# Performance work log

Measured on AMD Instinct MI355X. Metric: run time of the kernel, lower is better.

## Reference

```python
import jax, jax.numpy as jnp
import numpy as np
from jax import lax

B, T, D = 2, 2048, 2048
H, DK, DV = 16, 128, 128
K = 4  # conv kernel size
KEY_DIM = H * DK      # 2048
VAL_DIM = H * DV      # 2048
CONV_DIM = 2 * KEY_DIM + VAL_DIM  # 6144
EPS = 1e-6


def setup_inputs() -> dict:
    key = jax.random.key(0)
    ks = jax.random.split(key, 10)
    s = lambda fan: 1.0 / np.sqrt(fan)
    return {
        "hidden_states": jax.random.normal(ks[0], (B, T, D), jnp.float32),
        "W_qkv": jax.random.normal(ks[1], (D, CONV_DIM), jnp.float32) * s(D),
        "conv_w": jax.random.normal(ks[2], (CONV_DIM, 1, K), jnp.float32) * s(K),
        "W_z": jax.random.normal(ks[3], (D, VAL_DIM), jnp.float32) * s(D),
        "W_b": jax.random.normal(ks[4], (D, H), jnp.float32) * s(D),
        "W_a": jax.random.normal(ks[5], (D, H), jnp.float32) * s(D),
        "dt_bias": jnp.ones((H,), jnp.float32),
        "A_log": jnp.log(jax.random.uniform(ks[6], (H,), jnp.float32, 1e-3, 16.0)),
        "norm_weight": jnp.ones((DV,), jnp.float32),
        "W_out": jax.random.normal(ks[7], (VAL_DIM, D), jnp.float32) * s(VAL_DIM),
    }


def _l2norm(x):
    return x * lax.rsqrt(jnp.sum(x * x, axis=-1, keepdims=True) + 1e-6)


def _gated_delta_rule(q, k, v, g, beta):
    """q,k: [B,T,H,DK]; v: [B,T,H,DV]; g,beta: [B,T,H]. Returns o: [B,T,H,DV]."""
    # time-major for scan
    qT, kT, vT = (jnp.moveaxis(x, 1, 0) for x in (q, k, v))  # [T,B,H,d]
    gT = jnp.moveaxis(g, 1, 0)      # [T,B,H]
    bT = jnp.moveaxis(beta, 1, 0)   # [T,B,H]

    def step(S, inp):
        q_t, k_t, v_t, g_t, b_t = inp
        S = S * jnp.exp(g_t)[..., None, None]                      # decay [B,H,DK,DV]
        kv_mem = jnp.einsum("bhk,bhkv->bhv", k_t, S)               # S^T k
        delta = (v_t - kv_mem) * b_t[..., None]                     # beta-scaled error
        S = S + jnp.einsum("bhk,bhv->bhkv", k_t, delta)
        o_t = jnp.einsum("bhk,bhkv->bhv", q_t, S)
        return S, o_t

    S0 = jnp.zeros((q.shape[0], H, DK, DV), q.dtype)
    _, oT = lax.scan(step, S0, (qT, kT, vT, gT, bT))
    return jnp.moveaxis(oT, 0, 1)  # [B,T,H,DV]


def reference(hidden_states, W_qkv, conv_w, W_z, W_b, W_a, dt_bias, A_log,
              norm_weight, W_out):
    Bs, Ts, _ = hidden_states.shape

    # qkv projection + depthwise causal conv1d + silu
    mixed = hidden_states @ W_qkv                      # [B,T,CONV_DIM]
    xc = jnp.moveaxis(mixed, 1, 2)                     # [B,C,T]
    xc = lax.conv_general_dilated(xc, conv_w, (1,), [(K - 1, 0)],
                                  feature_group_count=CONV_DIM)
    mixed = jax.nn.silu(jnp.moveaxis(xc, 1, 2))        # [B,T,C]

    q, k, v = jnp.split(mixed, [KEY_DIM, 2 * KEY_DIM], axis=-1)
    q = _l2norm(q.reshape(Bs, Ts, H, DK)) * (DK ** -0.5)
    k = _l2norm(k.reshape(Bs, Ts, H, DK))
    v = v.reshape(Bs, Ts, H, DV)

    beta = jax.nn.sigmoid(hidden_states @ W_b)                     # [B,T,H]
    g = -jnp.exp(A_log) * jax.nn.softplus(hidden_states @ W_a + dt_bias)

    o = _gated_delta_rule(q, k, v, g, beta)            # [B,T,H,DV]

    # gated RMSNorm (Mamba2-style: gate first, then normalize)
    z = (hidden_states @ W_z).reshape(Bs, Ts, H, DV)
    o = o * jax.nn.silu(z)
    var = jnp.mean(o * o, axis=-1, keepdims=True)
    o = o * lax.rsqrt(var + EPS) * norm_weight

    return o.reshape(Bs, Ts, VAL_DIM) @ W_out          # [B,T,D]
```

## Files before the change

### kernel.cpp

```cpp
#include <hip/hip_runtime.h>

#define B_ 2
#define T_ 2048
#define D_ 2048
#define H_ 16
#define CONV_DIM_ 6144
#define NC_ 32
#define CK_ 64

typedef __bf16 bf16;
typedef bf16 bf16x8 __attribute__((ext_vector_type(8)));
typedef bf16 bf16x4 __attribute__((ext_vector_type(4)));
typedef float floatx4 __attribute__((ext_vector_type(4)));

__device__ __forceinline__ void async_copy16(bf16* lds, const bf16* g) {
    auto* g1 = (const __attribute__((address_space(1))) unsigned int*)g;
    auto* l3 = (__attribute__((address_space(3))) unsigned int*)lds;
    __builtin_amdgcn_global_load_lds(g1, l3, 16, 0, 0);
}

__global__ void cvt_bf16_kernel(const float* __restrict__ in, bf16* __restrict__ out, int n4) {
    int i = blockIdx.x * 256 + threadIdx.x;
    if (i < n4) {
        float4 v = ((const float4*)in)[i];
        bf16x4 o = { (bf16)v.x, (bf16)v.y, (bf16)v.z, (bf16)v.w };
        *(bf16x4*)(out + 4 * (size_t)i) = o;
    }
}

__global__ void transpose_kernel(const float* __restrict__ in, bf16* __restrict__ out, int R, int Cn) {
    __shared__ float tile[32][33];
    const int c0 = blockIdx.x << 5, r0 = blockIdx.y << 5;
    const int tx = threadIdx.x & 31, ty = threadIdx.x >> 5;
#pragma unroll
    for (int i = 0; i < 4; ++i) {
        int r = ty + (i << 3);
        tile[r][tx] = in[(size_t)(r0 + r) * Cn + c0 + tx];
    }
    __syncthreads();
#pragma unroll
    for (int i = 0; i < 4; ++i) {
        int cc = ty + (i << 3);
        out[(size_t)(c0 + cc) * R + r0 + tx] = (bf16)tile[tx][cc];
    }
}

__global__ void wba_cvt_kernel(const float* __restrict__ Wb, const float* __restrict__ Wa,
                               bf16* __restrict__ Wba) {
    int idx = blockIdx.x * 256 + threadIdx.x;
    int d = idx >> 4, h = idx & 15;
    Wba[(size_t)h * 2048 + d]        = (bf16)Wb[idx];
    Wba[(size_t)(h + 16) * 2048 + d] = (bf16)Wa[idx];
}

template <typename OutT>
__global__ __launch_bounds__(256) void gemm_kernel(
    const bf16* __restrict__ A, const bf16* __restrict__ Bt, OutT* __restrict__ C,
    int M, int N, int K) {
    __shared__ bf16 As[128 * 64];
    __shared__ bf16 Bs[128 * 64];
    const int tid = threadIdx.x;
    const int m0 = blockIdx.y << 7;
    const int n0 = blockIdx.x << 7;
    const int wave = tid >> 6, lane = tid & 63;
    const int wm = (wave >> 1) << 6, wn = (wave & 1) << 6;
    const int lrow = lane & 15, quad = lane >> 4;
    const int rl = lane >> 3;
    const int c8s = (lane & 7) ^ (rl & 7);

    floatx4 acc[4][4];
#pragma unroll
    for (int mt = 0; mt < 4; ++mt)
#pragma unroll
        for (int nt = 0; nt < 4; ++nt)
            acc[mt][nt] = floatx4{0.f, 0.f, 0.f, 0.f};

    for (int k0 = 0; k0 < K; k0 += 64) {
        __syncthreads();
#pragma unroll
        for (int i = 0; i < 4; ++i) {
            const int slot = wave * 4 + i;
            const int r = slot * 8 + rl;
            async_copy16(&As[slot * 512], A + (size_t)(m0 + r) * K + k0 + c8s * 8);
            async_copy16(&Bs[slot * 512], Bt + (size_t)(n0 + r) * K + k0 + c8s * 8);
        }
        __syncthreads();
#pragma unroll
        for (int kk = 0; kk < 64; kk += 32) {
            const int sw = (((kk >> 3) + quad) ^ (lrow & 7)) << 3;
            bf16x8 af[4], bfr[4];
#pragma unroll
            for (int mt = 0; mt < 4; ++mt) {
                af[mt]  = *(const bf16x8*)(&As[((wm + (mt << 4) + lrow) << 6) + sw]);
                bfr[mt] = *(const bf16x8*)(&Bs[((wn + (mt << 4) + lrow) << 6) + sw]);
            }
#pragma unroll
            for (int mt = 0; mt < 4; ++mt)
#pragma unroll
                for (int nt = 0; nt < 4; ++nt)
                    acc[mt][nt] = __builtin_amdgcn_mfma_f32_16x16x32_bf16(af[mt], bfr[nt], acc[mt][nt], 0, 0, 0);
        }
    }
#pragma unroll
    for (int mt = 0; mt < 4; ++mt)
#pragma unroll
        for (int nt = 0; nt < 4; ++nt) {
            const int col = n0 + wn + (nt << 4) + lrow;
            const int rowb = m0 + wm + (mt << 4) + (quad << 2);
#pragma unroll
            for (int i2 = 0; i2 < 4; ++i2)
                C[(size_t)(rowb + i2) * N + col] = (OutT)acc[mt][nt][i2];
        }
}

__global__ void conv_silu_kernel(const bf16* __restrict__ mixed, const float* __restrict__ cw,
                                 bf16* __restrict__ qb, bf16* __restrict__ kb, bf16* __restrict__ vb) {
    const int s = blockIdx.x;
    const int bt = blockIdx.y;
    const int t = bt & (T_ - 1);
    const int b = bt >> 11;
    const int c = (s << 7) + threadIdx.x;
    const size_t base = (size_t)bt * CONV_DIM_ + c;
    const float w0 = cw[c * 4], w1 = cw[c * 4 + 1], w2 = cw[c * 4 + 2], w3 = cw[c * 4 + 3];
    float acc = (float)mixed[base] * w3;
    if (t >= 1) acc += (float)mixed[base - CONV_DIM_] * w2;
    if (t >= 2) acc += (float)mixed[base - 2 * CONV_DIM_] * w1;
    if (t >= 3) acc += (float)mixed[base - 3 * CONV_DIM_] * w0;
    const float val = acc / (1.f + __expf(-acc));

    __shared__ float red[2];
    if (s < 32) {
        float ss = val * val;
#pragma unroll
        for (int o = 1; o < 64; o <<= 1) ss += __shfl_xor(ss, o);
        if ((threadIdx.x & 63) == 0) red[threadIdx.x >> 6] = ss;
        __syncthreads();
        const float scale = rsqrtf(red[0] + red[1] + 1e-6f);
        const int h = s & 15;
        const size_t oidx = (((size_t)(b * H_ + h)) * T_ + t) * 128 + threadIdx.x;
        if (s < 16) qb[oidx] = (bf16)(val * scale * 0.08838834764831845f);
        else        kb[oidx] = (bf16)(val * scale);
    } else {
        const int h = s - 32;
        const size_t oidx = (((size_t)(b * H_ + h)) * T_ + t) * 128 + threadIdx.x;
        vb[oidx] = (bf16)val;
    }
}

__global__ __launch_bounds__(256) void gbeta_mfma_kernel(
    const bf16* __restrict__ Xb, const bf16* __restrict__ Wba,
    const float* __restrict__ dtb, const float* __restrict__ Alog,
    float* __restrict__ gbuf, float* __restrict__ bbuf) {
    const int tid = threadIdx.x, wave = tid >> 6, lane = tid & 63;
    const int ln = lane & 15, qd = lane >> 4;
    const int m0 = blockIdx.x * 64 + wave * 16;
    floatx4 acc0 = {0.f, 0.f, 0.f, 0.f}, acc1 = {0.f, 0.f, 0.f, 0.f};
    const bf16* arow = Xb + (size_t)(m0 + ln) * 2048 + qd * 8;
    const bf16* b0 = Wba + (size_t)ln * 2048 + qd * 8;
    const bf16* b1 = Wba + (size_t)(16 + ln) * 2048 + qd * 8;
    for (int k = 0; k < 2048; k += 32) {
        bf16x8 af  = *(const bf16x8*)(arow + k);
        bf16x8 bf0 = *(const bf16x8*)(b0 + k);
        bf16x8 bf1 = *(const bf16x8*)(b1 + k);
        acc0 = __builtin_amdgcn_mfma_f32_16x16x32_bf16(af, bf0, acc0, 0, 0, 0);
        acc1 = __builtin_amdgcn_mfma_f32_16x16x32_bf16(af, bf1, acc1, 0, 0, 0);
    }
    const float dtbv = dtb[ln], al = __expf(Alog[ln]);
#pragma unroll
    for (int ii = 0; ii < 4; ++ii) {
        const int row = m0 + qd * 4 + ii;
        const int t = row & (T_ - 1), b = row >> 11;
        const size_t o = ((size_t)(b * H_ + ln)) * T_ + t;
        bbuf[o] = 1.f / (1.f + __expf(-acc0[ii]));
        const float xx = acc1[ii] + dtbv;
        const float sp = (xx > 15.f) ? xx : log1pf(__expf(xx));
        gbuf[o] = -al * sp;
    }
}

__global__ __launch_bounds__(256) void qkkt_kernel(const bf16* __restrict__ qb, const bf16* __restrict__ kb,
                                                   float* __restrict__ Araw, float* __restrict__ Mraw) {
    const int u = blockIdx.x;
    const int bh = u >> 5, nc = u & 31;
    const int t0 = nc * CK_;
    const int tid = threadIdx.x, wave = tid >> 6, lane = tid & 63;
    const int qd = lane >> 4, ln = lane & 15;
    __shared__ bf16 Kc[64 * 136], Qc[64 * 136];
    const size_t kbase = ((size_t)bh * T_ + t0) * 128;
#pragma unroll
    for (int it = 0; it < 4; ++it) {
        int idx = it * 256 + tid;
        int row = idx >> 4, c8 = idx & 15;
        *(uint4*)(&Kc[row * 136 + c8 * 8]) = *(const uint4*)(kb + kbase + row * 128 + c8 * 8);
        *(uint4*)(&Qc[row * 136 + c8 * 8]) = *(const uint4*)(qb + kbase + row * 128 + c8 * 8);
    }
    __syncthreads();
#pragma unroll
    for (int nt = 0; nt < 4; ++nt) {
        floatx4 accA = {0.f, 0.f, 0.f, 0.f}, accM = {0.f, 0.f, 0.f, 0.f};
#pragma unroll
        for (int kk = 0; kk < 4; ++kk) {
            bf16x8 bfr = *(const bf16x8*)(&Kc[(nt * 16 + ln) * 136 + kk * 32 + qd * 8]);
            bf16x8 afK = *(const bf16x8*)(&Kc[(wave * 16 + ln) * 136 + kk * 32 + qd * 8]);
            bf16x8 afQ = *(const bf16x8*)(&Qc[(wave * 16 + ln) * 136 + kk * 32 + qd * 8]);
            accA = __builtin_amdgcn_mfma_f32_16x16x32_bf16(afK, bfr, accA, 0, 0, 0);
            accM = __builtin_amdgcn_mfma_f32_16x16x32_bf16(afQ, bfr, accM, 0, 0, 0);
        }
#pragma unroll
        for (int ii = 0; ii < 4; ++ii) {
            int i = wave * 16 + qd * 4 + ii, j = nt * 16 + ln;
            Araw[(size_t)u * 4096 + i * 64 + j] = accA[ii];
            Mraw[(size_t)u * 4096 + i * 64 + j] = accM[ii];
        }
    }
}

__global__ __launch_bounds__(64) void prep_kernel(
    const float* __restrict__ gbuf, const float* __restrict__ bbuf,
    const float* __restrict__ Araw, const float* __restrict__ Mraw,
    float* __restrict__ lamg, float* __restrict__ ratiog,
    bf16* __restrict__ Tg, bf16* __restrict__ Mg) {
    const int u = blockIdx.x, bh = u >> 5, nc = u & 31, t0 = nc * CK_;
    const int lane = threadIdx.x;
    __shared__ float L[64 * 65];
    __shared__ float cv[64], bv[64];
    float g = gbuf[(size_t)bh * T_ + t0 + lane];
    float beta = bbuf[(size_t)bh * T_ + t0 + lane];
    float c = g;
#pragma unroll
    for (int off = 1; off < 64; off <<= 1) {
        float tval = __shfl_up(c, off);
        if (lane >= off) c += tval;
    }
    float c63 = __shfl(c, 63);
    lamg[(size_t)u * 64 + lane] = __expf(c);
    ratiog[(size_t)u * 64 + lane] = __expf(c63 - c);
    cv[lane] = c; bv[lane] = beta;
    __syncthreads();
    for (int i = 0; i < 64; ++i) {
        float a = Araw[(size_t)u * 4096 + i * 64 + lane];
        L[i * 65 + lane] = (lane < i) ? bv[i] * __expf(cv[i] - c) * a : 0.f;
    }
    __syncthreads();
    float t[64];
#pragma unroll
    for (int i = 0; i < 64; ++i) t[i] = (i == lane) ? 1.f : 0.f;
#pragma unroll
    for (int j = 0; j < 63; ++j) {
#pragma unroll
        for (int i = j + 1; i < 64; ++i)
            t[i] -= L[i * 65 + j] * t[j];
    }
#pragma unroll
    for (int i = 0; i < 64; ++i)
        Tg[(size_t)u * 4096 + i * 64 + lane] = (bf16)t[i];
    for (int i = 0; i < 64; ++i) {
        float m = Mraw[(size_t)u * 4096 + i * 64 + lane];
        float mij = (lane <= i) ? __expf(cv[i] - c) * m : 0.f;
        Mg[(size_t)u * 4096 + i * 64 + lane] = (bf16)mij;
    }
}

struct Pref {
    uint4 t2[2], m2[2];
    bf16x8 kf[4], qf[4];
    bf16x8 ktf[2][2];
    float rrv[4], vv[4], lam[4], bet[4], lamlast;
};

__device__ __forceinline__ void load_pref(
    Pref& p, int u, int t0, size_t kbase, int tid, int wave, int ln, int qd,
    int bh, int vbase,
    const bf16* __restrict__ qb, const bf16* __restrict__ kb, const bf16* __restrict__ vb,
    const bf16* __restrict__ Tg, const bf16* __restrict__ Mg,
    const float* __restrict__ lamg, const float* __restrict__ ratiog,
    const float* __restrict__ bbuf) {
#pragma unroll
    for (int it = 0; it < 2; ++it) {
        int idx = it * 256 + tid;
        int row = idx >> 3, c8 = idx & 7;
        p.t2[it] = *(const uint4*)(Tg + (size_t)u * 4096 + row * 64 + c8 * 8);
        p.m2[it] = *(const uint4*)(Mg + (size_t)u * 4096 + row * 64 + c8 * 8);
    }
    const size_t rowoff = kbase + (size_t)(wave * 16 + ln) * 128;
#pragma unroll
    for (int kk = 0; kk < 4; ++kk) {
        p.kf[kk] = *(const bf16x8*)(kb + rowoff + kk * 32 + qd * 8);
        p.qf[kk] = *(const bf16x8*)(qb + rowoff + kk * 32 + qd * 8);
    }
#pragma unroll
    for (int mt = 0; mt < 2; ++mt) {
        const int kd = (wave * 2 + mt) * 16 + ln;
#pragma unroll
        for (int kk2 = 0; kk2 < 2; ++kk2) {
            const int ib = kk2 * 32 + qd * 8;
#pragma unroll
            for (int j = 0; j < 8; ++j)
                p.ktf[mt][kk2][j] = kb[kbase + (size_t)(ib + j) * 128 + kd];
        }
    }
    const int i0 = wave * 16 + qd * 4;
#pragma unroll
    for (int ii = 0; ii < 4; ++ii) {
        p.vv[ii]  = (float)vb[kbase + (size_t)(i0 + ii) * 128 + vbase + ln];
        p.lam[ii] = lamg[(size_t)u * 64 + i0 + ii];
        p.bet[ii] = bbuf[(size_t)bh * T_ + t0 + i0 + ii];
        p.rrv[ii] = ratiog[(size_t)u * 64 + i0 + ii];
    }
    p.lamlast = lamg[(size_t)u * 64 + 63];
}

__global__ __launch_bounds__(256) void seq_kernel(
    const bf16* __restrict__ qb, const bf16* __restrict__ kb, const bf16* __restrict__ vb,
    const bf16* __restrict__ Tg, const bf16* __restrict__ Mg,
    const float* __restrict__ lamg, const float* __restrict__ ratiog,
    const float* __restrict__ bbuf, float* __restrict__ ob) {
    const int bh = blockIdx.x & 31;
    const int vs = blockIdx.x >> 5;
    const int vbase = vs * 16;
    const int tid = threadIdx.x;
    const int wave = tid >> 6, lane = tid & 63;
    const int qd = lane >> 4, ln = lane & 15;

    __shared__ bf16 Tt[64 * 72], Mm[64 * 72];
    __shared__ bf16 bT[16 * 72], Dt[16 * 72], Dtr[16 * 72];
    __shared__ bf16 Sbf[16 * 136];
    __shared__ float Sf[16 * 132];

    for (int idx = tid; idx < 16 * 132; idx += 256) Sf[idx] = 0.f;
    for (int idx = tid; idx < 16 * 136; idx += 256) Sbf[idx] = (bf16)0.f;

    Pref cur, nxt;
    load_pref(cur, bh * NC_, 0, (size_t)bh * T_ * 128, tid, wave, ln, qd, bh, vbase,
              qb, kb, vb, Tg, Mg, lamg, ratiog, bbuf);
    __syncthreads();

    for (int nc = 0; nc < NC_; ++nc) {
        const int t0 = nc * CK_;
        const size_t kbase = ((size_t)bh * T_ + t0) * 128;

#pragma unroll
        for (int it = 0; it < 2; ++it) {
            int idx = it * 256 + tid;
            int row = idx >> 3, c8 = idx & 7;
            *(uint4*)(&Tt[row * 72 + c8 * 8]) = cur.t2[it];
            *(uint4*)(&Mm[row * 72 + c8 * 8]) = cur.m2[it];
        }

        {
            const int ncn = (nc + 1 < NC_) ? nc + 1 : nc;
            load_pref(nxt, bh * NC_ + ncn, ncn * CK_, ((size_t)bh * T_ + (size_t)ncn * CK_) * 128,
                      tid, wave, ln, qd, bh, vbase, qb, kb, vb, Tg, Mg, lamg, ratiog, bbuf);
        }

        floatx4 ks = {0.f, 0.f, 0.f, 0.f};
#pragma unroll
        for (int kk = 0; kk < 4; ++kk) {
            bf16x8 bf = *(const bf16x8*)(&Sbf[ln * 136 + kk * 32 + qd * 8]);
            ks = __builtin_amdgcn_mfma_f32_16x16x32_bf16(cur.kf[kk], bf, ks, 0, 0, 0);
        }
        {
            const int i0 = wave * 16 + qd * 4;
            bf16x4 bw;
#pragma unroll
            for (int ii = 0; ii < 4; ++ii)
                bw[ii] = (bf16)(cur.bet[ii] * (cur.vv[ii] - cur.lam[ii] * ks[ii]));
            *(bf16x4*)(&bT[ln * 72 + i0]) = bw;
        }
        __syncthreads();

        {
            floatx4 acc = {0.f, 0.f, 0.f, 0.f};
#pragma unroll
            for (int kk = 0; kk < 2; ++kk) {
                bf16x8 af = *(const bf16x8*)(&Tt[(wave * 16 + ln) * 72 + kk * 32 + qd * 8]);
                bf16x8 bf = *(const bf16x8*)(&bT[ln * 72 + kk * 32 + qd * 8]);
                acc = __builtin_amdgcn_mfma_f32_16x16x32_bf16(af, bf, acc, 0, 0, 0);
            }
            const int i0 = wave * 16 + qd * 4;
            bf16x4 dw = { (bf16)acc[0], (bf16)acc[1], (bf16)acc[2], (bf16)acc[3] };
            *(bf16x4*)(&Dt[ln * 72 + i0]) = dw;
            bf16x4 dwr = { (bf16)(acc[0] * cur.rrv[0]), (bf16)(acc[1] * cur.rrv[1]),
                           (bf16)(acc[2] * cur.rrv[2]), (bf16)(acc[3] * cur.rrv[3]) };
            *(bf16x4*)(&Dtr[ln * 72 + i0]) = dwr;
        }
        __syncthreads();

        {
            floatx4 acc = {0.f, 0.f, 0.f, 0.f};
#pragma unroll
            for (int kk = 0; kk < 4; ++kk) {
                bf16x8 bf = *(const bf16x8*)(&Sbf[ln * 136 + kk * 32 + qd * 8]);
                acc = __builtin_amdgcn_mfma_f32_16x16x32_bf16(cur.qf[kk], bf, acc, 0, 0, 0);
            }
            floatx4 o;
#pragma unroll
            for (int ii = 0; ii < 4; ++ii) o[ii] = acc[ii] * cur.lam[ii];
#pragma unroll
            for (int kk = 0; kk < 2; ++kk) {
                bf16x8 af = *(const bf16x8*)(&Mm[(wave * 16 + ln) * 72 + kk * 32 + qd * 8]);
                bf16x8 bf = *(const bf16x8*)(&Dt[ln * 72 + kk * 32 + qd * 8]);
                o = __builtin_amdgcn_mfma_f32_16x16x32_bf16(af, bf, o, 0, 0, 0);
            }
            const int i0 = wave * 16 + qd * 4;
#pragma unroll
            for (int ii = 0; ii < 4; ++ii)
                ob[kbase + (size_t)(i0 + ii) * 128 + vbase + ln] = o[ii];
        }
#pragma unroll
        for (int mt = 0; mt < 2; ++mt) {
            const int kt = wave * 2 + mt;
            floatx4 acc = {0.f, 0.f, 0.f, 0.f};
#pragma unroll
            for (int kk = 0; kk < 2; ++kk) {
                bf16x8 bf = *(const bf16x8*)(&Dtr[ln * 72 + kk * 32 + qd * 8]);
                acc = __builtin_amdgcn_mfma_f32_16x16x32_bf16(cur.ktf[mt][kk], bf, acc, 0, 0, 0);
            }
            const int k0 = kt * 16 + qd * 4;
            floatx4 sold = *(floatx4*)(&Sf[ln * 132 + k0]);
#pragma unroll
            for (int ii = 0; ii < 4; ++ii) sold[ii] = sold[ii] * cur.lamlast + acc[ii];
            *(floatx4*)(&Sf[ln * 132 + k0]) = sold;
        }
        __syncthreads();
        {
            const int vloc = tid >> 4, k0 = (tid & 15) * 8;
            floatx4 s0 = *(floatx4*)(&Sf[vloc * 132 + k0]);
            floatx4 s1 = *(floatx4*)(&Sf[vloc * 132 + k0 + 4]);
            bf16x8 sb = { (bf16)s0[0], (bf16)s0[1], (bf16)s0[2], (bf16)s0[3],
                          (bf16)s1[0], (bf16)s1[1], (bf16)s1[2], (bf16)s1[3] };
            *(bf16x8*)(&Sbf[vloc * 136 + k0]) = sb;
        }
        __syncthreads();
        cur = nxt;
    }
}

__global__ void gated_norm_kernel(const float* __restrict__ ob, const bf16* __restrict__ z,
                                  const float* __restrict__ nw, bf16* __restrict__ onorm) {
    const int idx = blockIdx.x;
    const int h = idx & (H_ - 1);
    const int bt = idx >> 4;
    const int t = bt & (T_ - 1);
    const int b = bt >> 11;
    const int tid = threadIdx.x;
    const size_t obase = (((size_t)(b * H_ + h)) * T_ + t) * 128;
    const size_t zbase = (size_t)bt * 2048 + (h << 7);
    float o1 = ob[obase + tid], o2 = ob[obase + tid + 64];
    const float z1 = (float)z[zbase + tid], z2 = (float)z[zbase + tid + 64];
    o1 *= z1 / (1.f + __expf(-z1));
    o2 *= z2 / (1.f + __expf(-z2));
    float ss = o1 * o1 + o2 * o2;
#pragma unroll
    for (int o = 1; o < 64; o <<= 1) ss += __shfl_xor(ss, o);
    const float scale = rsqrtf(ss * (1.f / 128.f) + 1e-6f);
    onorm[zbase + tid]      = (bf16)(o1 * scale * nw[tid]);
    onorm[zbase + tid + 64] = (bf16)(o2 * scale * nw[tid + 64]);
}

extern "C" void kernel_launch(void* const* d_in, const int* in_sizes, int n_in,
                              void* d_out, int out_size, void* d_ws, size_t ws_size,
                              hipStream_t stream) {
    const float* X    = (const float*)d_in[0];
    const float* Wqkv = (const float*)d_in[1];
    const float* cw   = (const float*)d_in[2];
    const float* Wz   = (const float*)d_in[3];
    const float* Wb   = (const float*)d_in[4];
    const float* Wa   = (const float*)d_in[5];
    const float* dtb  = (const float*)d_in[6];
    const float* Alog = (const float*)d_in[7];
    const float* nw   = (const float*)d_in[8];
    const float* Wout = (const float*)d_in[9];
    float* out = (float*)d_out;

    char* ws = (char*)d_ws;
    size_t off = 0;
    auto alloc = [&](size_t bytes) -> char* {
        char* p = ws + off;
        off += (bytes + 255) & ~(size_t)255;
        return p;
    };
    bf16*  Xb      = (bf16*)alloc((size_t)B_ * T_ * D_ * 2);
    char*  wqkvt_p = alloc((size_t)CONV_DIM_ * D_ * 2);
    bf16*  Wqkvt   = (bf16*)wqkvt_p;
    bf16*  Wzt     = (bf16*)alloc((size_t)D_ * D_ * 2);
    bf16*  Woutt   = (bf16*)alloc((size_t)D_ * D_ * 2);
    bf16*  Wba     = (bf16*)alloc((size_t)32 * 2048 * 2);
    char*  mixed_p = alloc((size_t)B_ * T_ * CONV_DIM_ * 2);
    bf16*  mixedb  = (bf16*)mixed_p;
    bf16*  zb      = (bf16*)alloc((size_t)B_ * T_ * D_ * 2);
    bf16*  kbuf    = (bf16*)alloc((size_t)B_ * T_ * D_ * 2);
    bf16*  vbuf    = (bf16*)alloc((size_t)B_ * T_ * D_ * 2);
    float* gbuf    = (float*)alloc((size_t)B_ * T_ * H_ * 4);
    float* bbuf    = (float*)alloc((size_t)B_ * T_ * H_ * 4);
    float* Mraw    = (float*)alloc((size_t)1024 * 4096 * 4);
    bf16*  Tg      = (bf16*)alloc((size_t)1024 * 4096 * 2);
    bf16*  Mg      = (bf16*)alloc((size_t)1024 * 4096 * 2);
    float* lamg    = (float*)alloc((size_t)1024 * 64 * 4);
    float* ratiog  = (float*)alloc((size_t)1024 * 64 * 4);
    bf16*  qbuf    = (bf16*)wqkvt_p;
    float* obuf    = (float*)mixed_p;
    float* Araw    = (float*)(mixed_p + (size_t)B_ * T_ * D_ * 4);
    bf16*  onorm   = (bf16*)Xb;

    cvt_bf16_kernel<<<dim3((B_ * T_ * D_ / 4 + 255) / 256), dim3(256), 0, stream>>>(X, Xb, B_ * T_ * D_ / 4);
    transpose_kernel<<<dim3(CONV_DIM_ / 32, D_ / 32), dim3(256), 0, stream>>>(Wqkv, Wqkvt, D_, CONV_DIM_);
    transpose_kernel<<<dim3(D_ / 32, D_ / 32), dim3(256), 0, stream>>>(Wz, Wzt, D_, D_);
    transpose_kernel<<<dim3(D_ / 32, D_ / 32), dim3(256), 0, stream>>>(Wout, Woutt, D_, D_);
    wba_cvt_kernel<<<dim3(128), dim3(256), 0, stream>>>(Wb, Wa, Wba);

    gemm_kernel<bf16><<<dim3(CONV_DIM_ / 128, B_ * T_ / 128), dim3(256), 0, stream>>>(
        Xb, Wqkvt, mixedb, B_ * T_, CONV_DIM_, D_);
    gemm_kernel<bf16><<<dim3(D_ / 128, B_ * T_ / 128), dim3(256), 0, stream>>>(
        Xb, Wzt, zb, B_ * T_, D_, D_);

    gbeta_mfma_kernel<<<dim3(64), dim3(256), 0, stream>>>(Xb, Wba, dtb, Alog, gbuf, bbuf);
    conv_silu_kernel<<<dim3(CONV_DIM_ / 128, B_ * T_), dim3(128), 0, stream>>>(mixedb, cw, qbuf, kbuf, vbuf);

    qkkt_kernel<<<dim3(1024), dim3(256), 0, stream>>>(qbuf, kbuf, Araw, Mraw);
    prep_kernel<<<dim3(1024), dim3(64), 0, stream>>>(gbuf, bbuf, Araw, Mraw, lamg, ratiog, Tg, Mg);
    seq_kernel<<<dim3(256), dim3(256), 0, stream>>>(qbuf, kbuf, vbuf, Tg, Mg, lamg, ratiog, bbuf, obuf);

    gated_norm_kernel<<<dim3(B_ * T_ * H_), dim3(64), 0, stream>>>(obuf, zb, nw, onorm);

    gemm_kernel<float><<<dim3(D_ / 128, B_ * T_ / 128), dim3(256), 0, stream>>>(
        onorm, Woutt, out, B_ * T_, D_, D_);
}
```

Baseline: 666.7 us.

## Merge QKV and Z projections into one 256x256-tiled double-buffered GEMM

The two input projection GEMMs (QKV and Z) are replaced by a single GEMM over a concatenated transposed weight of width 8192. The new kernel uses 256x256 tiles with 512 threads and double-buffered async global-to-LDS loads. Epilogue stores are routed to either the mixed buffer or the z buffer depending on the column block. The larger tiles raise arithmetic intensity and cut launches, but they use more LDS and registers, which could lower occupancy. The grid is also smaller, 32x16 blocks.

```diff
diff --git a/kernel.cpp b/kernel.cpp
--- a/kernel.cpp
+++ b/kernel.cpp
@@ -110,6 +110,101 @@
 #pragma unroll
             for (int i2 = 0; i2 < 4; ++i2)
                 C[(size_t)(rowb + i2) * N + col] = (OutT)acc[mt][nt][i2];
+        }
+}
+
+__global__ __launch_bounds__(512, 2) void gemm256_kernel(
+    const bf16* __restrict__ A, const bf16* __restrict__ Bt,
+    bf16* __restrict__ C0, bf16* __restrict__ C1,
+    int M, int Ncat, int K, int split, int ld0, int ld1) {
+    __shared__ bf16 As[2][256 * 64];
+    __shared__ bf16 Bs[2][256 * 64];
+    const int tid = threadIdx.x;
+    const int wave = tid >> 6, lane = tid & 63;
+    const int quad = lane >> 4, lrow = lane & 15;
+    const int wm = (wave >> 2) << 7;
+    const int wn = (wave & 3) << 6;
+    const int m0 = blockIdx.y << 8, n0 = blockIdx.x << 8;
+
+    const int srow = tid >> 3;
+    const int cu_src = (tid & 7) ^ (srow & 7);
+    const bf16* ga[4];
+    const bf16* gb[4];
+#pragma unroll
+    for (int i = 0; i < 4; ++i) {
+        ga[i] = A  + (size_t)(m0 + i * 64 + srow) * K + cu_src * 8;
+        gb[i] = Bt + (size_t)(n0 + i * 64 + srow) * K + cu_src * 8;
+    }
+
+    floatx4 acc[8][4];
+#pragma unroll
+    for (int mt = 0; mt < 8; ++mt)
+#pragma unroll
+        for (int nt = 0; nt < 4; ++nt)
+            acc[mt][nt] = floatx4{0.f, 0.f, 0.f, 0.f};
+
+    const int KT = K >> 6;
+    auto stage = [&](int b, int kt) {
+        const int k0 = kt << 6;
+#pragma unroll
+        for (int i = 0; i < 4; ++i) {
+            async_copy16(&As[b][i * 4096 + wave * 512], ga[i] + k0);
+            async_copy16(&Bs[b][i * 4096 + wave * 512], gb[i] + k0);
+        }
+    };
+    stage(0, 0);
+    stage(1, 1);
+
+    for (int kt = 0; kt < KT; ++kt) {
+        if (kt + 1 < KT) asm volatile("s_waitcnt vmcnt(8)" ::: "memory");
+        else             asm volatile("s_waitcnt vmcnt(0)" ::: "memory");
+        __builtin_amdgcn_sched_barrier(0);
+        __builtin_amdgcn_s_barrier();
+        __builtin_amdgcn_sched_barrier(0);
+        const bf16* as = &As[kt & 1][0];
+        const bf16* bs = &Bs[kt & 1][0];
+#pragma unroll
+        for (int kk = 0; kk < 2; ++kk) {
+            const int sw = (((kk << 2) + quad) ^ (lrow & 7)) << 3;
+            bf16x8 bfr[4];
+#pragma unroll
+            for (int nt = 0; nt < 4; ++nt)
+                bfr[nt] = *(const bf16x8*)(bs + ((wn + nt * 16 + lrow) << 6) + sw);
+#pragma unroll
+            for (int mh = 0; mh < 2; ++mh) {
+                bf16x8 af[4];
+#pragma unroll
+                for (int mt = 0; mt < 4; ++mt)
+                    af[mt] = *(const bf16x8*)(as + ((wm + (mh * 4 + mt) * 16 + lrow) << 6) + sw);
+                __builtin_amdgcn_s_setprio(1);
+#pragma unroll
+                for (int mt = 0; mt < 4; ++mt)
+#pragma unroll
+                    for (int nt = 0; nt < 4; ++nt)
+                        acc[mh * 4 + mt][nt] = __builtin_amdgcn_mfma_f32_16x16x32_bf16(
+                            af[mt], bfr[nt], acc[mh * 4 + mt][nt], 0, 0, 0);
+                __builtin_amdgcn_s_setprio(0);
+            }
+        }
+        __builtin_amdgcn_sched_barrier(0);
+        __builtin_amdgcn_s_barrier();
+        __builtin_amdgcn_sched_barrier(0);
+        if (kt + 2 < KT) stage(kt & 1, kt + 2);
+    }
+
+    const bool second = (n0 >= split);
+    bf16* Cp = second ? C1 : C0;
+    const int ldc = second ? ld1 : ld0;
+    const int nc0 = second ? n0 - split : n0;
+#pragma unroll
+    for (int mt = 0; mt < 8; ++mt)
+#pragma unroll
+        for (int nt = 0; nt < 4; ++nt) {
+            const int col = nc0 + wn + nt * 16 + lrow;
+            const int rowb = m0 + wm + mt * 16 + (quad << 2);
+#pragma unroll
+            for (int i2 = 0; i2 < 4; ++i2)
+                Cp[(size_t)(rowb + i2) * ldc + col] = (bf16)acc[mt][nt][i2];
         }
 }
 
@@ -481,9 +576,8 @@
         return p;
     };
     bf16*  Xb      = (bf16*)alloc((size_t)B_ * T_ * D_ * 2);
-    char*  wqkvt_p = alloc((size_t)CONV_DIM_ * D_ * 2);
-    bf16*  Wqkvt   = (bf16*)wqkvt_p;
-    bf16*  Wzt     = (bf16*)alloc((size_t)D_ * D_ * 2);
+    char*  wcat_p  = alloc((size_t)8192 * 2048 * 2);
+    bf16*  Wcat    = (bf16*)wcat_p;
     bf16*  Woutt   = (bf16*)alloc((size_t)D_ * D_ * 2);
     bf16*  Wba     = (bf16*)alloc((size_t)32 * 2048 * 2);
     char*  mixed_p = alloc((size_t)B_ * T_ * CONV_DIM_ * 2);
@@ -498,21 +592,19 @@
     bf16*  Mg      = (bf16*)alloc((size_t)1024 * 4096 * 2);
     float* lamg    = (float*)alloc((size_t)1024 * 64 * 4);
     float* ratiog  = (float*)alloc((size_t)1024 * 64 * 4);
-    bf16*  qbuf    = (bf16*)wqkvt_p;
+    bf16*  qbuf    = (bf16*)wcat_p;
     float* obuf    = (float*)mixed_p;
     float* Araw    = (float*)(mixed_p + (size_t)B_ * T_ * D_ * 4);
     bf16*  onorm   = (bf16*)Xb;
 
     cvt_bf16_kernel<<<dim3((B_ * T_ * D_ / 4 + 255) / 256), dim3(256), 0, stream>>>(X, Xb, B_ * T_ * D_ / 4);
-    transpose_kernel<<<dim3(CONV_DIM_ / 32, D_ / 32), dim3(256), 0, stream>>>(Wqkv, Wqkvt, D_, CONV_DIM_);
-    transpose_kernel<<<dim3(D_ / 32, D_ / 32), dim3(256), 0, stream>>>(Wz, Wzt, D_, D_);
+    transpose_kernel<<<dim3(CONV_DIM_ / 32, D_ / 32), dim3(256), 0, stream>>>(Wqkv, Wcat, D_, CONV_DIM_);
+    transpose_kernel<<<dim3(D_ / 32, D_ / 32), dim3(256), 0, stream>>>(Wz, Wcat + (size_t)CONV_DIM_ * D_, D_, D_);
     transpose_kernel<<<dim3(D_ / 32, D_ / 32), dim3(256), 0, stream>>>(Wout, Woutt, D_, D_);
     wba_cvt_kernel<<<dim3(128), dim3(256), 0, stream>>>(Wb, Wa, Wba);
 
-    gemm_kernel<bf16><<<dim3(CONV_DIM_ / 128, B_ * T_ / 128), dim3(256), 0, stream>>>(
-        Xb, Wqkvt, mixedb, B_ * T_, CONV_DIM_, D_);
-    gemm_kernel<bf16><<<dim3(D_ / 128, B_ * T_ / 128), dim3(256), 0, stream>>>(
-        Xb, Wzt, zb, B_ * T_, D_, D_);
+    gemm256_kernel<<<dim3(8192 / 256, B_ * T_ / 256), dim3(512), 0, stream>>>(
+        Xb, Wcat, mixedb, zb, B_ * T_, 8192, D_, CONV_DIM_, CONV_DIM_, D_);
 
     gbeta_mfma_kernel<<<dim3(64), dim3(256), 0, stream>>>(Xb, Wba, dtb, Alog, gbuf, bbuf);
     conv_silu_kernel<<<dim3(CONV_DIM_ / 128, B_ * T_), dim3(128), 0, stream>>>(mixedb, cw, qbuf, kbuf, vbuf);
```

Result: faster. 645.1 us (-3.2%).
